# Kernel optimization log

Hardware: AMD Instinct MI355X
Metric: run time of the kernel (lower is better)

## Reference

```python
import jax, jax.numpy as jnp
from jax import lax
import numpy as np

B, L, I, H, W, O = 256, 1024, 16, 128, 512, 4


def _linear_init(key, fan_in, fan_out):
    # mimic torch nn.Linear default: U(-1/sqrt(fan_in), 1/sqrt(fan_in))
    kw, kb = jax.random.split(key)
    lim = 1.0 / np.sqrt(fan_in)
    Wm = jax.random.uniform(kw, (fan_in, fan_out), jnp.float32, -lim, lim)
    b = jax.random.uniform(kb, (fan_out,), jnp.float32, -lim, lim)
    return Wm, b


def setup_inputs() -> dict:
    key = jax.random.key(0)
    ks = jax.random.split(key, 10)
    # strictly increasing time grid: cumsum of small positive steps
    dts = jax.random.uniform(ks[0], (B, L), jnp.float32, 0.001, 0.01)
    ts = jnp.cumsum(dts, axis=1)
    x = jax.random.normal(ks[1], (B, L, I), jnp.float32)
    Wi1, bi1 = _linear_init(ks[2], I, W)
    Wi2, bi2 = _linear_init(ks[3], W, H)
    Wf1, bf1 = _linear_init(ks[4], H, W)
    Wf2, bf2 = _linear_init(ks[5], W, W)
    Wf3, bf3 = _linear_init(ks[6], W, H * I)
    Wo1, bo1 = _linear_init(ks[7], H, 32)
    Wo2, bo2 = _linear_init(ks[8], 32, O)
    return {"ts": ts, "x": x,
            "Wi1": Wi1, "bi1": bi1, "Wi2": Wi2, "bi2": bi2,
            "Wf1": Wf1, "bf1": bf1, "Wf2": Wf2, "bf2": bf2,
            "Wf3": Wf3, "bf3": bf3,
            "Wo1": Wo1, "bo1": bo1, "Wo2": Wo2, "bo2": bo2}


def reference(ts, x, Wi1, bi1, Wi2, bi2, Wf1, bf1, Wf2, bf2, Wf3, bf3, Wo1, bo1, Wo2, bo2):
    Bq, Lq, Iq = x.shape
    Hq = Wi2.shape[1]
    # initial network: y0 = Linear(tanh(Linear(x0)))
    y0 = jnp.tanh(x[:, 0, :] @ Wi1 + bi1) @ Wi2 + bi2  # (B, H)
    # precompute per-step increments as scan inputs
    dts = (ts[:, 1:] - ts[:, :-1]).T                      # (L-1, B)
    dxs = jnp.transpose(x[:, 1:, :] - x[:, :-1, :], (1, 0, 2))  # (L-1, B, I)

    def step(y, inp):
        dt, dx = inp  # (B,), (B, I)
        h = jnp.tanh(y @ Wf1 + bf1)
        h = jnp.tanh(h @ Wf2 + bf2)
        f = (h @ Wf3 + bf3).reshape(Bq, Hq, Iq)  # vector field (B, H, I)
        dy = jnp.einsum('bij,bj->bi', f, dx)
        return y + dy * dt[:, None], None

    yT, _ = lax.scan(step, y0, (dts, dxs))
    # output head with sigmoid
    out = jax.nn.sigmoid(jnp.tanh(yT @ Wo1 + bo1) @ Wo2 + bo2)  # (B, O)
    return out
```

## Files before the change

### kernel.cpp

```cpp
#include <hip/hip_runtime.h>


constexpr int LQ = 1024, IQ = 16, HQ = 128, WQ = 512, OQ = 4;
constexpr int THREADS = 512;
constexpr size_t CSTRIDE = 49152;

typedef __attribute__((ext_vector_type(8))) short bf16x8;
typedef __attribute__((ext_vector_type(4))) float f32x4;
typedef unsigned int u32t;
typedef unsigned long long u64t;

#define MFMA16(a, b, c) __builtin_amdgcn_mfma_f32_16x16x32_bf16((a), (b), (c), 0, 0, 0)

__device__ __forceinline__ unsigned short f2bf(float f) {
  unsigned u = __builtin_bit_cast(unsigned, f);
  u += 0x7FFFu + ((u >> 16) & 1u);
  return (unsigned short)(u >> 16);
}
__device__ __forceinline__ float bf2f(unsigned short h) {
  unsigned u = ((unsigned)h) << 16;
  return __builtin_bit_cast(float, u);
}
__device__ __forceinline__ float fast_tanh(float x) {
  float e = __expf(2.0f * x);
  return 1.0f - 2.0f / (e + 1.0f);
}
__device__ __forceinline__ u32t cvtpk(float lo, float hi) {
  u32t r;
  asm("v_cvt_pk_bf16_f32 %0, %1, %2" : "=v"(r) : "v"(lo), "v"(hi));
  return r;
}

__device__ __forceinline__ bf16x8 load_bfrag(const float* W, int N, int k0, int n0, int lane) {
  const int col = n0 + (lane & 15);
  const int kb  = k0 + 8 * (lane >> 4);
  bf16x8 v;
#pragma unroll
  for (int j = 0; j < 8; ++j) v[j] = (short)f2bf(W[(kb + j) * N + col]);
  return v;
}

__device__ __forceinline__ void st32a(u32t* p, u32t v) {
  __hip_atomic_store(p, v, __ATOMIC_RELAXED, __HIP_MEMORY_SCOPE_AGENT);
}
__device__ __forceinline__ u32t ld32a(const u32t* p) {
  return __hip_atomic_load(p, __ATOMIC_RELAXED, __HIP_MEMORY_SCOPE_AGENT);
}
__device__ __forceinline__ void st64a(u64t* p, u64t v) {
  __hip_atomic_store(p, v, __ATOMIC_RELAXED, __HIP_MEMORY_SCOPE_AGENT);
}
__device__ __forceinline__ u64t ld64a(const u64t* p) {
  return __hip_atomic_load(p, __ATOMIC_RELAXED, __HIP_MEMORY_SCOPE_AGENT);
}
__device__ __forceinline__ void faddA(float* p, float v) {
  __hip_atomic_fetch_add(p, v, __ATOMIC_RELAXED, __HIP_MEMORY_SCOPE_AGENT);
}
__device__ __forceinline__ void pollge(const u32t* p, u32t want) {
  while (ld32a(p) < want) __builtin_amdgcn_s_sleep(2);
  asm volatile("" ::: "memory");
}
__device__ __forceinline__ void drain_all() { __builtin_amdgcn_s_waitcnt(0); }

constexpr int OFF_YS  = 0;
constexpr int OFF_H1  = 4352;
constexpr int OFF_RED = 20992;
constexpr int OFF_B1  = 37888;
constexpr int OFF_B2  = 39936;
constexpr int OFF_H2S = 40064;
constexpr int OFF_DX  = 41344;
constexpr int OFF_DT  = 42624;
constexpr int POOLSZ  = 42688;


__global__ __launch_bounds__(THREADS, 2) void cde_kernel(
    const float* __restrict__ ts,  const float* __restrict__ x,
    const float* __restrict__ Wi1, const float* __restrict__ bi1,
    const float* __restrict__ Wi2, const float* __restrict__ bi2,
    const float* __restrict__ Wf1, const float* __restrict__ bfv1,
    const float* __restrict__ Wf2, const float* __restrict__ bfv2,
    const float* __restrict__ Wf3, const float* __restrict__ bfv3,
    const float* __restrict__ Wo1, const float* __restrict__ bo1,
    const float* __restrict__ Wo2, const float* __restrict__ bo2,
    float* __restrict__ out, unsigned char* __restrict__ ws) {
  const int tid  = threadIdx.x;
  const int wave = tid >> 6;
  const int lane = tid & 63;
  const int bid  = blockIdx.x;
  const int c    = bid >> 4;
  const int r    = bid & 15;

  unsigned char* cb = ws + (size_t)c * CSTRIDE;
  float* dyb  = (float*)(cb + 512);
  float* y0b  = (float*)(cb + 33280);
  u32t*  fy   = (u32t*)(cb + 41472);

  __shared__ __align__(16) unsigned char pool[POOLSZ];
  auto y_s = (unsigned short(*)[136])(pool + OFF_YS);
  auto h1s = (unsigned short(*)[520])(pool + OFF_H1);
  auto red = (float(*)[16][33])(pool + OFF_RED);
  auto h2s = (unsigned short(*)[40])(pool + OFF_H2S);
  auto h0f = (float(*)[512])(pool);
  float* b1s = (float*)(pool + OFF_B1);
  float* b2s = (float*)(pool + OFF_B2);
  float* dxs = (float*)(pool + OFF_DX);
  float* dtl = (float*)(pool + OFF_DT);

  bf16x8 w1f[4][4];
#pragma unroll
  for (int n = 0; n < 4; ++n)
#pragma unroll
    for (int k4 = 0; k4 < 4; ++k4)
      w1f[n][k4] = load_bfrag(Wf1, WQ, 32 * k4, 64 * wave + 16 * n, lane);
  const int w_nt = wave & 1, w_q = wave >> 1;
  bf16x8 w2f[4];
#pragma unroll
  for (int kk = 0; kk < 4; ++kk)
    w2f[kk] = load_bfrag(Wf2, WQ, 32 * (4 * w_q + kk), 32 * r + 16 * w_nt, lane);
  bf16x8 w3f[16];
  {
    const int h = 16 * wave + (lane & 15);
#pragma unroll
    for (int kk = 0; kk < 16; ++kk) {
      bf16x8 v;
#pragma unroll
      for (int jj = 0; jj < 8; ++jj) {
        int Kp = 32 * kk + 8 * (lane >> 4) + jj;
        int k = Kp >> 4, j = Kp & 15;
        v[jj] = (short)f2bf(Wf3[(32 * r + k) * (HQ * IQ) + 16 * h + j]);
      }
      w3f[kk] = v;
    }
  }
  bf16x8 w3b;
  {
    const int h = 16 * wave + (lane & 15);
    bf16x8 v;
#pragma unroll
    for (int jj = 0; jj < 8; ++jj) {
      int Kpp = 8 * (lane >> 4) + jj;
      v[jj] = (Kpp < 16) ? (short)f2bf(bfv3[16 * h + Kpp]) : (short)0;
    }
    w3b = v;
  }

  b1s[tid] = bi1[tid];
  if (tid < 32) b2s[tid] = bfv2[32 * r + tid];

  {
    int row = tid >> 5, col0 = (tid & 31) * 16;
    const float* xr = x + ((16 * c + row) * LQ) * IQ;
    float xv[16];
#pragma unroll
    for (int j = 0; j < 16; ++j) xv[j] = xr[j];
    for (int cc = 0; cc < 16; ++cc) {
      int col = col0 + cc;
      float s = bi1[col];
#pragma unroll
      for (int j = 0; j < 16; ++j) s += xv[j] * Wi1[j * WQ + col];
      h0f[row][col] = tanhf(s);
    }
  }
  __syncthreads();
  if (tid < 128) {
    int m = tid >> 3, hl = tid & 7;
    float s = bi2[8 * r + hl];
#pragma unroll 8
    for (int k = 0; k < WQ; ++k) s += h0f[m][k] * Wi2[k * HQ + 8 * r + hl];
    st32a((u32t*)&y0b[m * HQ + 8 * r + hl], __builtin_bit_cast(u32t, s));
  }
  drain_all();
  __syncthreads();
  if (tid == 0) st32a(fy + r, 1u);
  f32x4 y4;
  {
    pollge(fy + ((tid & 31) >> 1), 1u);
    u64t a = ld64a((const u64t*)(y0b + tid * 4));
    u64t b = ld64a((const u64t*)(y0b + tid * 4 + 2));
    y4[0] = __builtin_bit_cast(float, (u32t)a);
    y4[1] = __builtin_bit_cast(float, (u32t)(a >> 32));
    y4[2] = __builtin_bit_cast(float, (u32t)b);
    y4[3] = __builtin_bit_cast(float, (u32t)(b >> 32));
  }
  __syncthreads();

  const float* xrow = x + ((size_t)(16 * c + (tid >> 4))) * LQ * IQ + (tid & 15);
  const float* tsp  = ts + (size_t)(16 * c + tid) * LQ;

  for (int t = 0; t < LQ - 1; ++t) {
    const int A = t & 3;
    const u32t target = 16u * (u32t)((t >> 2) + 1);
    float* dyA = dyb + A * 2048;
    float* dyZ = dyb + ((t + 2) & 3) * 2048;
    u32t* cntA = (u32t*)(cb + A * 128);

    if (tid < 64) st64a((u64t*)(dyZ + r * 128 + tid * 2), 0ull);
    float xa = 0.f, xb = 0.f, ta = 0.f, tb = 0.f;
    if (tid < 256) { const float* xp = xrow + t * IQ; xa = xp[0]; xb = xp[IQ]; }
    if (tid < 16)  { ta = tsp[t]; tb = tsp[t + 1]; }
    {
      u32t w0 = cvtpk(y4[0], y4[1]), w1 = cvtpk(y4[2], y4[3]);
      *(u64t*)&y_s[tid >> 5][4 * (tid & 31)] = ((u64t)w1 << 32) | (u64t)w0;
    }
    __syncthreads();
    if (tid < 256) dxs[(tid >> 4) * 20 + (tid & 15)] = xb - xa;
    if (tid < 16)  dtl[tid] = tb - ta;
    {
      bf16x8 af[4];
#pragma unroll
      for (int k4 = 0; k4 < 4; ++k4)
        af[k4] = *(const bf16x8*)&y_s[lane & 15][32 * k4 + 8 * (lane >> 4)];
#pragma unroll
      for (int n = 0; n < 4; ++n) {
        f32x4 acc = {0.f, 0.f, 0.f, 0.f};
#pragma unroll
        for (int k4 = 0; k4 < 4; ++k4) acc = MFMA16(af[k4], w1f[n][k4], acc);
        const int col = 64 * wave + 16 * n + (lane & 15);
        const float bb = b1s[col];
#pragma unroll
        for (int i = 0; i < 4; ++i)
          h1s[4 * (lane >> 4) + i][col] = f2bf(fast_tanh(acc[i] + bb));
      }
    }
    __syncthreads();
    {
      f32x4 a0 = {0.f, 0.f, 0.f, 0.f}, a1 = {0.f, 0.f, 0.f, 0.f};
#pragma unroll
      for (int kk = 0; kk < 2; ++kk) {
        const bf16x8 f0 = *(const bf16x8*)&h1s[lane & 15][32 * (4 * w_q + kk) + 8 * (lane >> 4)];
        const bf16x8 f1 = *(const bf16x8*)&h1s[lane & 15][32 * (4 * w_q + kk + 2) + 8 * (lane >> 4)];
        a0 = MFMA16(f0, w2f[kk], a0);
        a1 = MFMA16(f1, w2f[kk + 2], a1);
      }
#pragma unroll
      for (int i = 0; i < 4; ++i)
        red[wave][4 * (lane >> 4) + i][lane & 15] = a0[i] + a1[i];
    }
    __syncthreads();
    if (tid < 256) {
      int row = tid >> 4, cp = tid & 15;
      int c0 = 2 * cp, c1 = c0 + 1, nt = cp >> 3, l0 = c0 & 15, l1 = c1 & 15;
      float v0 = b2s[c0], v1 = b2s[c1];
#pragma unroll
      for (int q = 0; q < 4; ++q) {
        v0 += red[(q << 1) | nt][row][l0];
        v1 += red[(q << 1) | nt][row][l1];
      }
      *(u32t*)&h2s[row][c0] = (u32t)f2bf(fast_tanh(v0)) | ((u32t)f2bf(fast_tanh(v1)) << 16);
    }
    __syncthreads();
    {
      const int b = lane & 15;
      u32t rd[16];
      {
        const uint4* hp = (const uint4*)&h2s[b][0];
        uint4 q0 = hp[0], q1 = hp[1], q2 = hp[2], q3 = hp[3];
        rd[0] = q0.x; rd[1] = q0.y; rd[2]  = q0.z; rd[3]  = q0.w;
        rd[4] = q1.x; rd[5] = q1.y; rd[6]  = q1.z; rd[7]  = q1.w;
        rd[8] = q2.x; rd[9] = q2.y; rd[10] = q2.z; rd[11] = q2.w;
        rd[12] = q3.x; rd[13] = q3.y; rd[14] = q3.z; rd[15] = q3.w;
      }
      float dxsel[8];
#pragma unroll
      for (int jj = 0; jj < 8; ++jj) {
        float lo = dxs[b * 20 + jj], hi = dxs[b * 20 + 8 + jj];
        dxsel[jj] = (lane & 16) ? hi : lo;
      }
      f32x4 acc = {0.f, 0.f, 0.f, 0.f};
#pragma unroll
      for (int kk = 0; kk < 16; ++kk) {
        u32t d = rd[kk];
        float ha = bf2f((unsigned short)(d & 0xffffu));
        float hb = bf2f((unsigned short)(d >> 16));
        float hv = (lane & 32) ? hb : ha;
        int4 ai;
        ai.x = (int)cvtpk(hv * dxsel[0], hv * dxsel[1]);
        ai.y = (int)cvtpk(hv * dxsel[2], hv * dxsel[3]);
        ai.z = (int)cvtpk(hv * dxsel[4], hv * dxsel[5]);
        ai.w = (int)cvtpk(hv * dxsel[6], hv * dxsel[7]);
        acc = MFMA16(__builtin_bit_cast(bf16x8, ai), w3f[kk], acc);
      }
      if (r == 0) {
        int4 bi4;
        if (lane & 32) {
          bi4.x = bi4.y = bi4.z = bi4.w = 0;
        } else {
          bi4.x = (int)cvtpk(dxsel[0], dxsel[1]);
          bi4.y = (int)cvtpk(dxsel[2], dxsel[3]);
          bi4.z = (int)cvtpk(dxsel[4], dxsel[5]);
          bi4.w = (int)cvtpk(dxsel[6], dxsel[7]);
        }
        acc = MFMA16(__builtin_bit_cast(bf16x8, bi4), w3b, acc);
      }
      const int g = lane >> 4, hcol = 16 * wave + b;
#pragma unroll
      for (int i = 0; i < 4; ++i)
        faddA(dyA + (4 * g + i) * HQ + hcol, acc[i]);
    }
    drain_all();
    __syncthreads();
    if (tid == 0) __hip_atomic_fetch_add(cntA, 1u, __ATOMIC_RELAXED, __HIP_MEMORY_SCOPE_AGENT);
    pollge(cntA, target);
    {
      u64t a = ld64a((const u64t*)(dyA + tid * 4));
      u64t b = ld64a((const u64t*)(dyA + tid * 4 + 2));
      const float dtv = dtl[tid >> 5];
      y4[0] += __builtin_bit_cast(float, (u32t)a) * dtv;
      y4[1] += __builtin_bit_cast(float, (u32t)(a >> 32)) * dtv;
      y4[2] += __builtin_bit_cast(float, (u32t)b) * dtv;
      y4[3] += __builtin_bit_cast(float, (u32t)(b >> 32)) * dtv;
    }
  }

  if (r == 0) {
    float* yf = (float*)(pool + OFF_RED);
    {
      int m = tid >> 5, h4 = 4 * (tid & 31);
#pragma unroll
      for (int i = 0; i < 4; ++i) yf[m * HQ + h4 + i] = y4[i];
    }
    __syncthreads();
    float* gep = (float*)(pool + OFF_YS);
    {
      int m = tid >> 5, o = tid & 31;
      float s = bo1[o];
#pragma unroll 8
      for (int k = 0; k < HQ; ++k) s += yf[m * HQ + k] * Wo1[k * 32 + o];
      gep[m * 32 + o] = tanhf(s);
    }
    __syncthreads();
    if (tid < 64) {
      int m = tid >> 2, oo = tid & 3;
      float s = bo2[oo];
#pragma unroll
      for (int k = 0; k < 32; ++k) s += gep[m * 32 + k] * Wo2[k * OQ + oo];
      out[(16 * c + m) * OQ + oo] = 1.f / (1.f + __expf(-s));
    }
  }
}

extern "C" void kernel_launch(void* const* d_in, const int* in_sizes, int n_in,
                              void* d_out, int out_size, void* d_ws, size_t ws_size,
                              hipStream_t stream) {
  (void)in_sizes; (void)n_in; (void)out_size; (void)ws_size;
  hipMemsetAsync(d_ws, 0, 16 * CSTRIDE, stream);
  cde_kernel<<<dim3(256), dim3(THREADS), 0, stream>>>(
      (const float*)d_in[0],  (const float*)d_in[1],
      (const float*)d_in[2],  (const float*)d_in[3],
      (const float*)d_in[4],  (const float*)d_in[5],
      (const float*)d_in[6],  (const float*)d_in[7],
      (const float*)d_in[8],  (const float*)d_in[9],
      (const float*)d_in[10], (const float*)d_in[11],
      (const float*)d_in[12], (const float*)d_in[13],
      (const float*)d_in[14], (const float*)d_in[15],
      (float*)d_out, (unsigned char*)d_ws);
}
```

Before: 6.570 ms.

## Split bf16 activations into hi/lo pairs and replace atomic adds with partial-sum slots

Activations y, h1 and the h2*dx products are now split into high and low bf16 parts, and each is multiplied with the bf16 weights. This roughly doubles the MFMA work per step in exchange for better accuracy. The cross-block reduction of dy no longer uses float atomic adds into a zeroed ring buffer. Each block writes its partial to its own slot, and every block sums all 16 slots after a double-buffered counter barrier. This also drops the per-step buffer zeroing, shortens the poll sleep and sets launch bounds to 1 block per CU because LDS grew.

Measured after the change: 10.16 ms (median of 5 runs). 54.7% more time.

```diff
diff --git a/kernel.cpp b/kernel.cpp
--- a/kernel.cpp
+++ b/kernel.cpp
@@ -3,7 +3,8 @@
 
 constexpr int LQ = 1024, IQ = 16, HQ = 128, WQ = 512, OQ = 4;
 constexpr int THREADS = 512;
-constexpr size_t CSTRIDE = 49152;
+constexpr size_t PCS   = 270336;
+constexpr size_t PBASE = 65536;
 
 typedef __attribute__((ext_vector_type(8))) short bf16x8;
 typedef __attribute__((ext_vector_type(4))) float f32x4;
@@ -30,6 +31,11 @@
   asm("v_cvt_pk_bf16_f32 %0, %1, %2" : "=v"(r) : "v"(lo), "v"(hi));
   return r;
 }
+__device__ __forceinline__ u32t lo_pair(float p0, float p1, u32t hpk) {
+  float h0 = __builtin_bit_cast(float, hpk << 16);
+  float h1 = __builtin_bit_cast(float, hpk & 0xffff0000u);
+  return cvtpk(p0 - h0, p1 - h1);
+}
 
 __device__ __forceinline__ bf16x8 load_bfrag(const float* W, int N, int k0, int n0, int lane) {
   const int col = n0 + (lane & 15);
@@ -46,33 +52,29 @@
 __device__ __forceinline__ u32t ld32a(const u32t* p) {
   return __hip_atomic_load(p, __ATOMIC_RELAXED, __HIP_MEMORY_SCOPE_AGENT);
 }
-__device__ __forceinline__ void st64a(u64t* p, u64t v) {
-  __hip_atomic_store(p, v, __ATOMIC_RELAXED, __HIP_MEMORY_SCOPE_AGENT);
-}
 __device__ __forceinline__ u64t ld64a(const u64t* p) {
   return __hip_atomic_load(p, __ATOMIC_RELAXED, __HIP_MEMORY_SCOPE_AGENT);
 }
-__device__ __forceinline__ void faddA(float* p, float v) {
-  __hip_atomic_fetch_add(p, v, __ATOMIC_RELAXED, __HIP_MEMORY_SCOPE_AGENT);
-}
 __device__ __forceinline__ void pollge(const u32t* p, u32t want) {
-  while (ld32a(p) < want) __builtin_amdgcn_s_sleep(2);
+  while (ld32a(p) < want) __builtin_amdgcn_s_sleep(1);
   asm volatile("" ::: "memory");
 }
 __device__ __forceinline__ void drain_all() { __builtin_amdgcn_s_waitcnt(0); }
 
-constexpr int OFF_YS  = 0;
-constexpr int OFF_H1  = 4352;
-constexpr int OFF_RED = 20992;
-constexpr int OFF_B1  = 37888;
-constexpr int OFF_B2  = 39936;
-constexpr int OFF_H2S = 40064;
-constexpr int OFF_DX  = 41344;
-constexpr int OFF_DT  = 42624;
-constexpr int POOLSZ  = 42688;
-
-
-__global__ __launch_bounds__(THREADS, 2) void cde_kernel(
+constexpr int OFF_YSH = 0;
+constexpr int OFF_YSL = 4352;
+constexpr int OFF_H1H = 8704;
+constexpr int OFF_H1L = 25344;
+constexpr int OFF_RED = 41984;
+constexpr int OFF_B1  = 58880;
+constexpr int OFF_B2  = 60928;
+constexpr int OFF_H2F = 61056;
+constexpr int OFF_DX  = 63168;
+constexpr int OFF_DT  = 64448;
+constexpr int POOLSZ  = 64512;
+
+
+__global__ __launch_bounds__(THREADS, 1) void cde_kernel(
     const float* __restrict__ ts,  const float* __restrict__ x,
     const float* __restrict__ Wi1, const float* __restrict__ bi1,
     const float* __restrict__ Wi2, const float* __restrict__ bi2,
@@ -89,17 +91,19 @@
   const int c    = bid >> 4;
   const int r    = bid & 15;
 
-  unsigned char* cb = ws + (size_t)c * CSTRIDE;
-  float* dyb  = (float*)(cb + 512);
-  float* y0b  = (float*)(cb + 33280);
-  u32t*  fy   = (u32t*)(cb + 41472);
+  u32t* cnt = (u32t*)(ws + (size_t)c * 256);
+  u32t* fy  = (u32t*)(ws + 8192 + (size_t)c * 64);
+  float* part = (float*)(ws + PBASE + (size_t)c * PCS);
+  float* y0b  = (float*)(ws + PBASE + (size_t)c * PCS + 262144);
 
   __shared__ __align__(16) unsigned char pool[POOLSZ];
-  auto y_s = (unsigned short(*)[136])(pool + OFF_YS);
-  auto h1s = (unsigned short(*)[520])(pool + OFF_H1);
-  auto red = (float(*)[16][33])(pool + OFF_RED);
-  auto h2s = (unsigned short(*)[40])(pool + OFF_H2S);
-  auto h0f = (float(*)[512])(pool);
+  auto y_sh = (unsigned short(*)[136])(pool + OFF_YSH);
+  auto y_sl = (unsigned short(*)[136])(pool + OFF_YSL);
+  auto h1h  = (unsigned short(*)[520])(pool + OFF_H1H);
+  auto h1l  = (unsigned short(*)[520])(pool + OFF_H1L);
+  auto red  = (float(*)[16][33])(pool + OFF_RED);
+  auto h2f  = (float(*)[33])(pool + OFF_H2F);
+  auto h0f  = (float(*)[512])(pool);
   float* b1s = (float*)(pool + OFF_B1);
   float* b2s = (float*)(pool + OFF_B2);
   float* dxs = (float*)(pool + OFF_DX);
@@ -183,42 +187,50 @@
   }
   __syncthreads();
 
+  const int g_row = tid >> 5, g_c4 = 4 * (tid & 31);
   const float* xrow = x + ((size_t)(16 * c + (tid >> 4))) * LQ * IQ + (tid & 15);
   const float* tsp  = ts + (size_t)(16 * c + tid) * LQ;
 
   for (int t = 0; t < LQ - 1; ++t) {
-    const int A = t & 3;
-    const u32t target = 16u * (u32t)((t >> 2) + 1);
-    float* dyA = dyb + A * 2048;
-    float* dyZ = dyb + ((t + 2) & 3) * 2048;
-    u32t* cntA = (u32t*)(cb + A * 128);
-
-    if (tid < 64) st64a((u64t*)(dyZ + r * 128 + tid * 2), 0ull);
+    const int par = t & 1;
+    u32t* cntP = cnt + par * 32;
+    float* slotW = part + (size_t)(par * 16 + r) * 2048;
+
     float xa = 0.f, xb = 0.f, ta = 0.f, tb = 0.f;
     if (tid < 256) { const float* xp = xrow + t * IQ; xa = xp[0]; xb = xp[IQ]; }
     if (tid < 16)  { ta = tsp[t]; tb = tsp[t + 1]; }
     {
-      u32t w0 = cvtpk(y4[0], y4[1]), w1 = cvtpk(y4[2], y4[3]);
-      *(u64t*)&y_s[tid >> 5][4 * (tid & 31)] = ((u64t)w1 << 32) | (u64t)w0;
+      u32t h0 = cvtpk(y4[0], y4[1]), h1 = cvtpk(y4[2], y4[3]);
+      u32t g0 = lo_pair(y4[0], y4[1], h0), g1 = lo_pair(y4[2], y4[3], h1);
+      *(u64t*)&y_sh[g_row][g_c4] = ((u64t)h1 << 32) | (u64t)h0;
+      *(u64t*)&y_sl[g_row][g_c4] = ((u64t)g1 << 32) | (u64t)g0;
     }
     __syncthreads();
     if (tid < 256) dxs[(tid >> 4) * 20 + (tid & 15)] = xb - xa;
     if (tid < 16)  dtl[tid] = tb - ta;
     {
-      bf16x8 af[4];
-#pragma unroll
-      for (int k4 = 0; k4 < 4; ++k4)
-        af[k4] = *(const bf16x8*)&y_s[lane & 15][32 * k4 + 8 * (lane >> 4)];
+      bf16x8 afh[4], afl[4];
+#pragma unroll
+      for (int k4 = 0; k4 < 4; ++k4) {
+        afh[k4] = *(const bf16x8*)&y_sh[lane & 15][32 * k4 + 8 * (lane >> 4)];
+        afl[k4] = *(const bf16x8*)&y_sl[lane & 15][32 * k4 + 8 * (lane >> 4)];
+      }
 #pragma unroll
       for (int n = 0; n < 4; ++n) {
         f32x4 acc = {0.f, 0.f, 0.f, 0.f};
 #pragma unroll
-        for (int k4 = 0; k4 < 4; ++k4) acc = MFMA16(af[k4], w1f[n][k4], acc);
+        for (int k4 = 0; k4 < 4; ++k4) acc = MFMA16(afh[k4], w1f[n][k4], acc);
+#pragma unroll
+        for (int k4 = 0; k4 < 4; ++k4) acc = MFMA16(afl[k4], w1f[n][k4], acc);
         const int col = 64 * wave + 16 * n + (lane & 15);
         const float bb = b1s[col];
 #pragma unroll
-        for (int i = 0; i < 4; ++i)
-          h1s[4 * (lane >> 4) + i][col] = f2bf(fast_tanh(acc[i] + bb));
+        for (int i = 0; i < 4; ++i) {
+          float hv = fast_tanh(acc[i] + bb);
+          unsigned short hh = f2bf(hv);
+          h1h[4 * (lane >> 4) + i][col] = hh;
+          h1l[4 * (lane >> 4) + i][col] = f2bf(hv - bf2f(hh));
+        }
       }
     }
     __syncthreads();
@@ -226,10 +238,12 @@
       f32x4 a0 = {0.f, 0.f, 0.f, 0.f}, a1 = {0.f, 0.f, 0.f, 0.f};
 #pragma unroll
       for (int kk = 0; kk < 2; ++kk) {
-        const bf16x8 f0 = *(const bf16x8*)&h1s[lane & 15][32 * (4 * w_q + kk) + 8 * (lane >> 4)];
-        const bf16x8 f1 = *(const bf16x8*)&h1s[lane & 15][32 * (4 * w_q + kk + 2) + 8 * (lane >> 4)];
-        a0 = MFMA16(f0, w2f[kk], a0);
-        a1 = MFMA16(f1, w2f[kk + 2], a1);
+        const int o0 = 32 * (4 * w_q + kk) + 8 * (lane >> 4);
+        const int o1 = 32 * (4 * w_q + kk + 2) + 8 * (lane >> 4);
+        a0 = MFMA16(*(const bf16x8*)&h1h[lane & 15][o0], w2f[kk], a0);
+        a0 = MFMA16(*(const bf16x8*)&h1l[lane & 15][o0], w2f[kk], a0);
+        a1 = MFMA16(*(const bf16x8*)&h1h[lane & 15][o1], w2f[kk + 2], a1);
+        a1 = MFMA16(*(const bf16x8*)&h1l[lane & 15][o1], w2f[kk + 2], a1);
       }
 #pragma unroll
       for (int i = 0; i < 4; ++i)
@@ -245,81 +259,84 @@
         v0 += red[(q << 1) | nt][row][l0];
         v1 += red[(q << 1) | nt][row][l1];
       }
-      *(u32t*)&h2s[row][c0] = (u32t)f2bf(fast_tanh(v0)) | ((u32t)f2bf(fast_tanh(v1)) << 16);
+      h2f[row][c0] = fast_tanh(v0);
+      h2f[row][c1] = fast_tanh(v1);
     }
     __syncthreads();
     {
       const int b = lane & 15;
-      u32t rd[16];
-      {
-        const uint4* hp = (const uint4*)&h2s[b][0];
-        uint4 q0 = hp[0], q1 = hp[1], q2 = hp[2], q3 = hp[3];
-        rd[0] = q0.x; rd[1] = q0.y; rd[2]  = q0.z; rd[3]  = q0.w;
-        rd[4] = q1.x; rd[5] = q1.y; rd[6]  = q1.z; rd[7]  = q1.w;
-        rd[8] = q2.x; rd[9] = q2.y; rd[10] = q2.z; rd[11] = q2.w;
-        rd[12] = q3.x; rd[13] = q3.y; rd[14] = q3.z; rd[15] = q3.w;
-      }
+      const int ksel = (lane >> 5) & 1;
       float dxsel[8];
 #pragma unroll
-      for (int jj = 0; jj < 8; ++jj) {
-        float lo = dxs[b * 20 + jj], hi = dxs[b * 20 + 8 + jj];
-        dxsel[jj] = (lane & 16) ? hi : lo;
-      }
+      for (int jj = 0; jj < 8; ++jj)
+        dxsel[jj] = dxs[b * 20 + ((lane & 16) ? 8 : 0) + jj];
+      float hvv[16];
+#pragma unroll
+      for (int kk = 0; kk < 16; ++kk) hvv[kk] = h2f[b][2 * kk + ksel];
       f32x4 acc = {0.f, 0.f, 0.f, 0.f};
 #pragma unroll
       for (int kk = 0; kk < 16; ++kk) {
-        u32t d = rd[kk];
-        float ha = bf2f((unsigned short)(d & 0xffffu));
-        float hb = bf2f((unsigned short)(d >> 16));
-        float hv = (lane & 32) ? hb : ha;
-        int4 ai;
-        ai.x = (int)cvtpk(hv * dxsel[0], hv * dxsel[1]);
-        ai.y = (int)cvtpk(hv * dxsel[2], hv * dxsel[3]);
-        ai.z = (int)cvtpk(hv * dxsel[4], hv * dxsel[5]);
-        ai.w = (int)cvtpk(hv * dxsel[6], hv * dxsel[7]);
-        acc = MFMA16(__builtin_bit_cast(bf16x8, ai), w3f[kk], acc);
+        const float hv = hvv[kk];
+        float p0 = hv * dxsel[0], p1 = hv * dxsel[1], p2 = hv * dxsel[2], p3 = hv * dxsel[3];
+        float p4 = hv * dxsel[4], p5 = hv * dxsel[5], p6 = hv * dxsel[6], p7 = hv * dxsel[7];
+        int4 hi, lo;
+        hi.x = (int)cvtpk(p0, p1); lo.x = (int)lo_pair(p0, p1, (u32t)hi.x);
+        hi.y = (int)cvtpk(p2, p3); lo.y = (int)lo_pair(p2, p3, (u32t)hi.y);
+        hi.z = (int)cvtpk(p4, p5); lo.z = (int)lo_pair(p4, p5, (u32t)hi.z);
+        hi.w = (int)cvtpk(p6, p7); lo.w = (int)lo_pair(p6, p7, (u32t)hi.w);
+        acc = MFMA16(__builtin_bit_cast(bf16x8, hi), w3f[kk], acc);
+        acc = MFMA16(__builtin_bit_cast(bf16x8, lo), w3f[kk], acc);
       }
       if (r == 0) {
-        int4 bi4;
+        int4 bh, bl;
         if (lane & 32) {
-          bi4.x = bi4.y = bi4.z = bi4.w = 0;
+          bh.x = bh.y = bh.z = bh.w = 0; bl = bh;
         } else {
-          bi4.x = (int)cvtpk(dxsel[0], dxsel[1]);
-          bi4.y = (int)cvtpk(dxsel[2], dxsel[3]);
-          bi4.z = (int)cvtpk(dxsel[4], dxsel[5]);
-          bi4.w = (int)cvtpk(dxsel[6], dxsel[7]);
+          bh.x = (int)cvtpk(dxsel[0], dxsel[1]); bl.x = (int)lo_pair(dxsel[0], dxsel[1], (u32t)bh.x);
+          bh.y = (int)cvtpk(dxsel[2], dxsel[3]); bl.y = (int)lo_pair(dxsel[2], dxsel[3], (u32t)bh.y);
+          bh.z = (int)cvtpk(dxsel[4], dxsel[5]); bl.z = (int)lo_pair(dxsel[4], dxsel[5], (u32t)bh.z);
+          bh.w = (int)cvtpk(dxsel[6], dxsel[7]); bl.w = (int)lo_pair(dxsel[6], dxsel[7], (u32t)bh.w);
         }
-        acc = MFMA16(__builtin_bit_cast(bf16x8, bi4), w3b, acc);
-      }
-      const int g = lane >> 4, hcol = 16 * wave + b;
+        acc = MFMA16(__builtin_bit_cast(bf16x8, bh), w3b, acc);
+        acc = MFMA16(__builtin_bit_cast(bf16x8, bl), w3b, acc);
+      }
+      const int hcol = 16 * wave + b;
 #pragma unroll
       for (int i = 0; i < 4; ++i)
-        faddA(dyA + (4 * g + i) * HQ + hcol, acc[i]);
+        st32a((u32t*)&slotW[(4 * (lane >> 4) + i) * 128 + hcol],
+              __builtin_bit_cast(u32t, acc[i]));
     }
     drain_all();
     __syncthreads();
-    if (tid == 0) __hip_atomic_fetch_add(cntA, 1u, __ATOMIC_RELAXED, __HIP_MEMORY_SCOPE_AGENT);
-    pollge(cntA, target);
-    {
-      u64t a = ld64a((const u64t*)(dyA + tid * 4));
-      u64t b = ld64a((const u64t*)(dyA + tid * 4 + 2));
-      const float dtv = dtl[tid >> 5];
-      y4[0] += __builtin_bit_cast(float, (u32t)a) * dtv;
-      y4[1] += __builtin_bit_cast(float, (u32t)(a >> 32)) * dtv;
-      y4[2] += __builtin_bit_cast(float, (u32t)b) * dtv;
-      y4[3] += __builtin_bit_cast(float, (u32t)(b >> 32)) * dtv;
+    if (tid == 0)
+      __hip_atomic_fetch_add(cntP, 1u, __ATOMIC_RELAXED, __HIP_MEMORY_SCOPE_AGENT);
+    pollge(cntP, 16u * (u32t)((t >> 1) + 1));
+    {
+      float s0 = 0.f, s1 = 0.f, s2 = 0.f, s3 = 0.f;
+#pragma unroll
+      for (int i = 0; i < 16; ++i) {
+        int rr = (r + i) & 15;
+        const float* pb = part + (size_t)(par * 16 + rr) * 2048 + g_row * 128 + g_c4;
+        u64t a = ld64a((const u64t*)pb);
+        u64t b = ld64a((const u64t*)(pb + 2));
+        s0 += __builtin_bit_cast(float, (u32t)a);
+        s1 += __builtin_bit_cast(float, (u32t)(a >> 32));
+        s2 += __builtin_bit_cast(float, (u32t)b);
+        s3 += __builtin_bit_cast(float, (u32t)(b >> 32));
+      }
+      const float dtv = dtl[g_row];
+      y4[0] += s0 * dtv; y4[1] += s1 * dtv; y4[2] += s2 * dtv; y4[3] += s3 * dtv;
     }
   }
 
   if (r == 0) {
     float* yf = (float*)(pool + OFF_RED);
     {
-      int m = tid >> 5, h4 = 4 * (tid & 31);
-#pragma unroll
-      for (int i = 0; i < 4; ++i) yf[m * HQ + h4 + i] = y4[i];
-    }
-    __syncthreads();
-    float* gep = (float*)(pool + OFF_YS);
+#pragma unroll
+      for (int i = 0; i < 4; ++i) yf[g_row * HQ + g_c4 + i] = y4[i];
+    }
+    __syncthreads();
+    float* gep = (float*)(pool + OFF_YSH);
     {
       int m = tid >> 5, o = tid & 31;
       float s = bo1[o];
@@ -342,7 +359,7 @@
                               void* d_out, int out_size, void* d_ws, size_t ws_size,
                               hipStream_t stream) {
   (void)in_sizes; (void)n_in; (void)out_size; (void)ws_size;
-  hipMemsetAsync(d_ws, 0, 16 * CSTRIDE, stream);
+  hipMemsetAsync(d_ws, 0, 65536, stream);
   cde_kernel<<<dim3(256), dim3(THREADS), 0, stream>>>(
       (const float*)d_in[0],  (const float*)d_in[1],
       (const float*)d_in[2],  (const float*)d_in[3],
```
